# Kernel tuning notes

Measured on AMD Instinct MI355X. Metric: run time of the kernel, lower is better.

Reference implementation:

```python
import jax, jax.numpy as jnp
import numpy as np
import math

D_MODEL = 1024
NUM_HEADS = 16
HEAD_DIM = D_MODEL // NUM_HEADS
REPETITIONS = 3
NEG = -10000.0


def setup_inputs() -> dict:
    key = jax.random.key(0)
    ks = jax.random.split(key, 5)
    B, S = 2, 2048
    x = jax.random.normal(ks[0], (B, S, D_MODEL), dtype=jnp.float32)
    Wqkv_w = jax.random.normal(ks[1], (3 * D_MODEL, D_MODEL), dtype=jnp.float32) * (1.0 / math.sqrt(D_MODEL))
    Wqkv_b = jax.random.normal(ks[2], (3 * D_MODEL,), dtype=jnp.float32) * 0.02
    out_w = jax.random.normal(ks[3], (D_MODEL, D_MODEL), dtype=jnp.float32) * (1.0 / math.sqrt(D_MODEL))
    out_b = jax.random.normal(ks[4], (D_MODEL,), dtype=jnp.float32) * 0.02
    return {"x": x, "Wqkv_w": Wqkv_w, "Wqkv_b": Wqkv_b, "out_w": out_w, "out_b": out_b}


def _self_attention(q, k, v, mask):
    # q,k,v: (B,S,H,D); mask: (S,S) additive causal (-10000 above diagonal)
    scale = 1.0 / math.sqrt(q.shape[-1])
    scores = jnp.einsum('bthd,bshd->bhts', q, k * scale) + mask  # (B,H,S,S)
    attn = jax.nn.softmax(scores, axis=-1)
    return jnp.einsum('bhts,bshd->bthd', attn, v)  # (B,S,H,D)


def reference(x, Wqkv_w, Wqkv_b, out_w, out_b):
    B, S, _ = x.shape
    qkv = x @ Wqkv_w.T + Wqkv_b                       # (B,S,3*D_MODEL)
    qkv = qkv.reshape(B, S, 3, NUM_HEADS, HEAD_DIM)
    q, k, v = qkv[:, :, 0], qkv[:, :, 1], qkv[:, :, 2]
    mask = jnp.triu(jnp.full((S, S), NEG, dtype=x.dtype), 1)
    context = _self_attention(q, k, v, mask)
    # recurrent re-attention: rep_dim == 'q' -> query replaced by previous context
    for _ in range(REPETITIONS - 1):
        context = _self_attention(context, k, v, mask)
    out = context.reshape(B, S, D_MODEL) @ out_w.T + out_b
    return out
```

## Files before the change

### kernel.cpp

```cpp
#include <hip/hip_runtime.h>


#define D_MODEL 1024
#define NHEADS  16
#define HD      64
#define SEQ     2048
#define BATCH   2
#define NROWS   (BATCH*SEQ)
#define NQKV    (3*D_MODEL)
#define SCL2F   0.1803368801111601f
#define MASK2   (-14426.950408889634f)

typedef __bf16 bf16x8 __attribute__((ext_vector_type(8)));
typedef float  f32x4  __attribute__((ext_vector_type(4)));
typedef unsigned short us8 __attribute__((ext_vector_type(8)));
typedef unsigned short us4 __attribute__((ext_vector_type(4)));
typedef short  s16x4  __attribute__((ext_vector_type(4)));

__device__ __forceinline__ unsigned short f2bf(float f) {
  unsigned int u = __float_as_uint(f);
  u = (u + 0x7fffu + ((u >> 16) & 1u)) >> 16;
  return (unsigned short)u;
}

union Pack8 { us8 v; unsigned short e[8]; };
union Pack4 { us4 v; unsigned short e[4]; };

__device__ __forceinline__ us8 cvt8(const float4 &a, const float4 &b) {
  Pack8 p;
  p.e[0]=f2bf(a.x); p.e[1]=f2bf(a.y); p.e[2]=f2bf(a.z); p.e[3]=f2bf(a.w);
  p.e[4]=f2bf(b.x); p.e[5]=f2bf(b.y); p.e[6]=f2bf(b.z); p.e[7]=f2bf(b.w);
  return p.v;
}

__device__ __forceinline__ void gl_lds16(const unsigned short* g, unsigned short* l) {
  __builtin_amdgcn_global_load_lds(
      (const __attribute__((address_space(1))) unsigned int*)g,
      (__attribute__((address_space(3))) unsigned int*)l, 16, 0, 0);
}

#define CVT_N1 (NROWS*D_MODEL)
#define CVT_N2 (NQKV*D_MODEL)
#define CVT_N3 (D_MODEL*D_MODEL)

__global__ __launch_bounds__(256) void cvt_all(
    const float* __restrict__ x, const float* __restrict__ wq,
    const float* __restrict__ ow,
    unsigned short* __restrict__ xb, unsigned short* __restrict__ wqb,
    unsigned short* __restrict__ owb)
{
  size_t i = ((size_t)blockIdx.x * 256 + threadIdx.x) * 8;
  const float* src; unsigned short* dst; size_t off;
  if (i < CVT_N1)                { src = x;  dst = xb;  off = i; }
  else if (i < CVT_N1 + CVT_N2)  { src = wq; dst = wqb; off = i - CVT_N1; }
  else                           { src = ow; dst = owb; off = i - CVT_N1 - CVT_N2; }
  float4 a = *(const float4*)(src + off);
  float4 b = *(const float4*)(src + off + 4);
  *(us8*)(dst + off) = cvt8(a, b);
}

__global__ __launch_bounds__(256) void qkv_gemm(
    const unsigned short* __restrict__ xb, const unsigned short* __restrict__ wqb,
    const float* __restrict__ bias,
    unsigned short* __restrict__ q, unsigned short* __restrict__ k,
    unsigned short* __restrict__ vT)
{
  __shared__ __align__(16) unsigned short As[128*64];
  __shared__ __align__(16) unsigned short Bs[128*64];
  const int tid = threadIdx.x;
  const int m0 = blockIdx.y * 128, n0 = blockIdx.x * 128;
  const int wave = tid >> 6, lane = tid & 63;
  const int wm = (wave >> 1) * 64, wn = (wave & 1) * 64;
  const int lrow = lane & 15, quad = lane >> 4;

  const int dr = lane >> 3;
  const int pg = lane & 7;
  const int sg = (pg ^ dr) * 8;
  const unsigned short* gA[4]; const unsigned short* gB[4];
  unsigned short *lA[4], *lB[4];
  #pragma unroll
  for (int i = 0; i < 4; i++) {
    int c = wave*4 + i;
    gA[i] = xb  + (size_t)(m0 + c*8 + dr) * D_MODEL + sg;
    gB[i] = wqb + (size_t)(n0 + c*8 + dr) * D_MODEL + sg;
    lA[i] = &As[c*512];
    lB[i] = &Bs[c*512];
  }
  const int px0 = (quad ^ (lrow & 7)) * 8;
  const int px1 = ((quad + 4) ^ (lrow & 7)) * 8;

  f32x4 acc[4][4];
  #pragma unroll
  for (int i = 0; i < 4; i++)
    #pragma unroll
    for (int j = 0; j < 4; j++) acc[i][j] = (f32x4){0.f,0.f,0.f,0.f};

  for (int k0 = 0; k0 < D_MODEL; k0 += 64) {
    __syncthreads();
    #pragma unroll
    for (int i = 0; i < 4; i++) { gl_lds16(gA[i] + k0, lA[i]); gl_lds16(gB[i] + k0, lB[i]); }
    __syncthreads();
    bf16x8 af[4][2], bfr[4][2];
    #pragma unroll
    for (int mf = 0; mf < 4; mf++) {
      int row = wm + mf*16 + lrow;
      af[mf][0] = *(const bf16x8*)&As[row*64 + px0];
      af[mf][1] = *(const bf16x8*)&As[row*64 + px1];
    }
    #pragma unroll
    for (int nb = 0; nb < 4; nb++) {
      int row = wn + nb*16 + lrow;
      bfr[nb][0] = *(const bf16x8*)&Bs[row*64 + px0];
      bfr[nb][1] = *(const bf16x8*)&Bs[row*64 + px1];
    }
    #pragma unroll
    for (int h = 0; h < 2; h++)
      #pragma unroll
      for (int mf = 0; mf < 4; mf++)
        #pragma unroll
        for (int nb = 0; nb < 4; nb++)
          acc[mf][nb] = __builtin_amdgcn_mfma_f32_16x16x32_bf16(af[mf][h], bfr[nb][h], acc[mf][nb], 0, 0, 0);
  }

  #pragma unroll
  for (int mf = 0; mf < 4; mf++) {
    #pragma unroll
    for (int nb = 0; nb < 4; nb++) {
      int n = n0 + wn + nb*16 + lrow;
      int which = n >> 10;
      int h  = (n >> 6) & 15;
      int hd = n & 63;
      int mb = m0 + wm + mf*16 + quad*4;
      int b  = mb >> 11;
      int s  = mb & 2047;
      float bi = bias[n];
      if (which == 2) {
        Pack4 p4;
        #pragma unroll
        for (int r = 0; r < 4; r++) p4.e[r] = f2bf(acc[mf][nb][r] + bi);
        *(us4*)&vT[((size_t)((b*NHEADS + h)*HD + hd))*SEQ + s] = p4.v;
      } else {
        unsigned short* dst = (which == 0) ? q : k;
        float scl = (which == 0) ? SCL2F : 1.0f;
        #pragma unroll
        for (int r = 0; r < 4; r++)
          dst[(size_t)((b*NHEADS + h)*SEQ + s + r)*HD + hd] = f2bf((acc[mf][nb][r] + bi) * scl);
      }
    }
  }
}

#define LDQ 80

__global__ __launch_bounds__(256) void attn3(
    const unsigned short* __restrict__ qg,
    const unsigned short* __restrict__ kg,
    const unsigned short* __restrict__ vTg,
    unsigned short* __restrict__ ctx)
{
  __shared__ __align__(16) unsigned short Ks[2][64*LDQ];
  __shared__ __align__(16) unsigned short Vs[2][64*LDQ];
  unsigned short* QC = &Vs[0][0];

  const int tid  = threadIdx.x;
  const int w    = tid >> 6, lane = tid & 63;
  const int lrow = lane & 15, quad = lane >> 4;
  const int bh = blockIdx.x;
  const int yy = blockIdx.y;
  const int base = (blockIdx.x + yy) & 7;
  const int qt = (yy < 8) ? base : (15 - base);
  const unsigned short* qbase = qg  + (size_t)bh * SEQ * HD;
  const unsigned short* kbase = kg  + (size_t)bh * SEQ * HD;
  const unsigned short* vbase = vTg + (size_t)bh * HD * SEQ;
  unsigned short* cbase = ctx + (size_t)bh * SEQ * HD;

  const int srow = tid >> 2;
  const int sco  = (tid & 3) * 16;
  const int qrow = tid >> 1, qc0 = (tid & 1) * 32;

  {
    const unsigned short* src = qbase + (size_t)(qt*128 + qrow)*HD + qc0;
    *(uint4*)&QC[qrow*LDQ + qc0]      = *(const uint4*)src;
    *(uint4*)&QC[qrow*LDQ + qc0 + 8]  = *(const uint4*)(src + 8);
    *(uint4*)&QC[qrow*LDQ + qc0 + 16] = *(const uint4*)(src + 16);
    *(uint4*)&QC[qrow*LDQ + qc0 + 24] = *(const uint4*)(src + 24);
  }
  __syncthreads();

  bf16x8 qb[2][2];
  #pragma unroll
  for (int qgi = 0; qgi < 2; qgi++) {
    qb[qgi][0] = *(const bf16x8*)&QC[(w*32 + qgi*16 + lrow)*LDQ + quad*8];
    qb[qgi][1] = *(const bf16x8*)&QC[(w*32 + qgi*16 + lrow)*LDQ + 32 + quad*8];
  }
  __syncthreads();

  const int kmax = 2*qt + 1;
  const int qwbase = qt*128 + w*32;

  for (int rep = 0; rep < 3; ++rep) {
    f32x4 od[2][4];
    #pragma unroll
    for (int qgi = 0; qgi < 2; qgi++)
      #pragma unroll
      for (int df = 0; df < 4; df++) od[qgi][df] = (f32x4){0.f,0.f,0.f,0.f};
    float ls[2] = {0.f, 0.f};

    uint4 kr0, kr1, vr0, vr1;
    {
      const unsigned short* ks = kbase + (size_t)srow*HD + sco;
      kr0 = *(const uint4*)ks;  kr1 = *(const uint4*)(ks + 8);
      const unsigned short* vs = vbase + (size_t)srow*SEQ + sco;
      vr0 = *(const uint4*)vs;  vr1 = *(const uint4*)(vs + 8);
    }

    for (int kt = 0; kt <= kmax; ++kt) {
      const int b = kt & 1;
      *(uint4*)&Ks[b][srow*LDQ + sco]     = kr0;
      *(uint4*)&Ks[b][srow*LDQ + sco + 8] = kr1;
      *(uint4*)&Vs[b][srow*LDQ + sco]     = vr0;
      *(uint4*)&Vs[b][srow*LDQ + sco + 8] = vr1;
      if (kt < kmax) {
        const unsigned short* ks = kbase + (size_t)((kt+1)*64 + srow)*HD + sco;
        kr0 = *(const uint4*)ks;  kr1 = *(const uint4*)(ks + 8);
        const unsigned short* vs = vbase + (size_t)srow*SEQ + (kt+1)*64 + sco;
        vr0 = *(const uint4*)vs;  vr1 = *(const uint4*)(vs + 8);
      }
      __syncthreads();

      const int sbase = kt*64;
      const bool skip = sbase > (qwbase + 31);
      if (!skip) {
        f32x4 sc[2][4];
        #pragma unroll
        for (int sf = 0; sf < 4; sf++) {
          bf16x8 a0 = *(const bf16x8*)&Ks[b][(sf*16 + lrow)*LDQ + quad*8];
          bf16x8 a1 = *(const bf16x8*)&Ks[b][(sf*16 + lrow)*LDQ + 32 + quad*8];
          f32x4 z0 = (f32x4){0.f,0.f,0.f,0.f}, z1 = z0;
          z0 = __builtin_amdgcn_mfma_f32_16x16x32_bf16(a0, qb[0][0], z0, 0, 0, 0);
          z1 = __builtin_amdgcn_mfma_f32_16x16x32_bf16(a0, qb[1][0], z1, 0, 0, 0);
          z0 = __builtin_amdgcn_mfma_f32_16x16x32_bf16(a1, qb[0][1], z0, 0, 0, 0);
          z1 = __builtin_amdgcn_mfma_f32_16x16x32_bf16(a1, qb[1][1], z1, 0, 0, 0);
          sc[0][sf] = z0; sc[1][sf] = z1;
        }
        if (sbase + 63 > qwbase) {
          #pragma unroll
          for (int qgi = 0; qgi < 2; qgi++) {
            int ql = qwbase + qgi*16 + lrow;
            #pragma unroll
            for (int sf = 0; sf < 4; sf++)
              #pragma unroll
              for (int r = 0; r < 4; r++)
                if (sbase + sf*16 + quad*4 + r > ql) sc[qgi][sf][r] += MASK2;
          }
        }
        s16x4 pf[2][4];
        #pragma unroll
        for (int qgi = 0; qgi < 2; qgi++) {
          float lp = 0.f;
          #pragma unroll
          for (int sf = 0; sf < 4; sf++) {
            Pack4 pk;
            #pragma unroll
            for (int r = 0; r < 4; r++) {
              float pe = __builtin_amdgcn_exp2f(sc[qgi][sf][r]);
              lp += pe;
              pk.e[r] = __builtin_bit_cast(unsigned short, (__bf16)pe);
            }
            pf[qgi][sf] = __builtin_bit_cast(s16x4, pk.v);
          }
          ls[qgi] += lp;
        }
        #pragma unroll
        for (int df = 0; df < 4; df++) {
          s16x4 v0 = *(const s16x4*)&Vs[b][(df*16 + lrow)*LDQ +  0 + quad*4];
          s16x4 v1 = *(const s16x4*)&Vs[b][(df*16 + lrow)*LDQ + 16 + quad*4];
          s16x4 v2 = *(const s16x4*)&Vs[b][(df*16 + lrow)*LDQ + 32 + quad*4];
          s16x4 v3 = *(const s16x4*)&Vs[b][(df*16 + lrow)*LDQ + 48 + quad*4];
          od[0][df] = __builtin_amdgcn_mfma_f32_16x16x16bf16_1k(v0, pf[0][0], od[0][df], 0, 0, 0);
          od[1][df] = __builtin_amdgcn_mfma_f32_16x16x16bf16_1k(v0, pf[1][0], od[1][df], 0, 0, 0);
          od[0][df] = __builtin_amdgcn_mfma_f32_16x16x16bf16_1k(v1, pf[0][1], od[0][df], 0, 0, 0);
          od[1][df] = __builtin_amdgcn_mfma_f32_16x16x16bf16_1k(v1, pf[1][1], od[1][df], 0, 0, 0);
          od[0][df] = __builtin_amdgcn_mfma_f32_16x16x16bf16_1k(v2, pf[0][2], od[0][df], 0, 0, 0);
          od[1][df] = __builtin_amdgcn_mfma_f32_16x16x16bf16_1k(v2, pf[1][2], od[1][df], 0, 0, 0);
          od[0][df] = __builtin_amdgcn_mfma_f32_16x16x16bf16_1k(v3, pf[0][3], od[0][df], 0, 0, 0);
          od[1][df] = __builtin_amdgcn_mfma_f32_16x16x16bf16_1k(v3, pf[1][3], od[1][df], 0, 0, 0);
        }
      }
    }

    #pragma unroll
    for (int qgi = 0; qgi < 2; qgi++) {
      ls[qgi] += __shfl_xor(ls[qgi], 16);
      ls[qgi] += __shfl_xor(ls[qgi], 32);
    }

    __syncthreads();
    #pragma unroll
    for (int qgi = 0; qgi < 2; qgi++) {
      float f = ((rep < 2) ? SCL2F : 1.0f) / ls[qgi];
      #pragma unroll
      for (int df = 0; df < 4; df++) {
        Pack4 pk;
        #pragma unroll
        for (int r = 0; r < 4; r++)
          pk.e[r] = __builtin_bit_cast(unsigned short, (__bf16)(od[qgi][df][r] * f));
        *(us4*)&QC[(w*32 + qgi*16 + lrow)*LDQ + df*16 + quad*4] = pk.v;
      }
    }
    __syncthreads();
    if (rep < 2) {
      #pragma unroll
      for (int qgi = 0; qgi < 2; qgi++) {
        qb[qgi][0] = *(const bf16x8*)&QC[(w*32 + qgi*16 + lrow)*LDQ + quad*8];
        qb[qgi][1] = *(const bf16x8*)&QC[(w*32 + qgi*16 + lrow)*LDQ + 32 + quad*8];
      }
      __syncthreads();
    }
  }

  {
    unsigned short* dst = cbase + (size_t)(qt*128 + qrow)*HD + qc0;
    *(uint4*)dst        = *(const uint4*)&QC[qrow*LDQ + qc0];
    *(uint4*)(dst + 8)  = *(const uint4*)&QC[qrow*LDQ + qc0 + 8];
    *(uint4*)(dst + 16) = *(const uint4*)&QC[qrow*LDQ + qc0 + 16];
    *(uint4*)(dst + 24) = *(const uint4*)&QC[qrow*LDQ + qc0 + 24];
  }
}

__global__ __launch_bounds__(256) void out_gemm(
    const unsigned short* __restrict__ ctx, const unsigned short* __restrict__ owb,
    const float* __restrict__ bias, float* __restrict__ out)
{
  __shared__ __align__(16) unsigned short As[128*64];
  __shared__ __align__(16) unsigned short Bs[64*64];
  const int tid = threadIdx.x;
  const int m0 = blockIdx.y * 128, n0 = blockIdx.x * 64;
  const int wave = tid >> 6, lane = tid & 63;
  const int wm = (wave >> 1) * 64, wn = (wave & 1) * 32;
  const int lrow = lane & 15, quad = lane >> 4;

  const int dr = lane >> 3, pg = lane & 7;
  const int sg = (pg ^ dr) * 8;
  size_t aoff[4]; unsigned short* lA[4];
  #pragma unroll
  for (int i = 0; i < 4; i++) {
    int c = wave*4 + i;
    int row = m0 + c*8 + dr;
    aoff[i] = ((size_t)((row >> 11)*NHEADS)*SEQ + (row & 2047))*HD + sg;
    lA[i] = &As[c*512];
  }
  const unsigned short* gB[2]; unsigned short* lB[2];
  #pragma unroll
  for (int j = 0; j < 2; j++) {
    int c = wave*2 + j;
    gB[j] = owb + (size_t)(n0 + c*8 + dr) * D_MODEL + sg;
    lB[j] = &Bs[c*512];
  }
  const int px0 = (quad ^ (lrow & 7)) * 8;
  const int px1 = ((quad + 4) ^ (lrow & 7)) * 8;

  f32x4 acc[4][2];
  #pragma unroll
  for (int i = 0; i < 4; i++)
    #pragma unroll
    for (int j = 0; j < 2; j++) acc[i][j] = (f32x4){0.f,0.f,0.f,0.f};

  for (int k0 = 0; k0 < D_MODEL; k0 += 64) {
    size_t hoff = (size_t)(k0 >> 6) * SEQ * HD;
    __syncthreads();
    #pragma unroll
    for (int i = 0; i < 4; i++) gl_lds16(ctx + aoff[i] + hoff, lA[i]);
    #pragma unroll
    for (int j = 0; j < 2; j++) gl_lds16(gB[j] + k0, lB[j]);
    __syncthreads();
    bf16x8 af[4][2], bfr[2][2];
    #pragma unroll
    for (int mf = 0; mf < 4; mf++) {
      int row = wm + mf*16 + lrow;
      af[mf][0] = *(const bf16x8*)&As[row*64 + px0];
      af[mf][1] = *(const bf16x8*)&As[row*64 + px1];
    }
    #pragma unroll
    for (int nb = 0; nb < 2; nb++) {
      int row = wn + nb*16 + lrow;
      bfr[nb][0] = *(const bf16x8*)&Bs[row*64 + px0];
      bfr[nb][1] = *(const bf16x8*)&Bs[row*64 + px1];
    }
    #pragma unroll
    for (int h = 0; h < 2; h++)
      #pragma unroll
      for (int mf = 0; mf < 4; mf++)
        #pragma unroll
        for (int nb = 0; nb < 2; nb++)
          acc[mf][nb] = __builtin_amdgcn_mfma_f32_16x16x32_bf16(af[mf][h], bfr[nb][h], acc[mf][nb], 0, 0, 0);
  }

  #pragma unroll
  for (int mf = 0; mf < 4; mf++) {
    #pragma unroll
    for (int nb = 0; nb < 2; nb++) {
      #pragma unroll
      for (int r = 0; r < 4; r++) {
        int mm = m0 + wm + mf*16 + quad*4 + r;
        int n  = n0 + wn + nb*16 + lrow;
        out[(size_t)mm * D_MODEL + n] = acc[mf][nb][r] + bias[n];
      }
    }
  }
}

extern "C" void kernel_launch(void* const* d_in, const int* in_sizes, int n_in,
                              void* d_out, int out_size, void* d_ws, size_t ws_size,
                              hipStream_t stream) {
  (void)in_sizes; (void)n_in; (void)out_size; (void)ws_size;
  const float* x      = (const float*)d_in[0];
  const float* Wqkv_w = (const float*)d_in[1];
  const float* Wqkv_b = (const float*)d_in[2];
  const float* out_w  = (const float*)d_in[3];
  const float* out_b  = (const float*)d_in[4];
  float* out = (float*)d_out;

  unsigned short* ws = (unsigned short*)d_ws;
  unsigned short* xb  = ws;
  unsigned short* wqb = ws + CVT_N1;
  unsigned short* owb = ws + CVT_N1 + CVT_N2;
  unsigned short* q   = ws + CVT_N1 + CVT_N2 + CVT_N3;
  unsigned short* k   = q + (size_t)NROWS*D_MODEL;
  unsigned short* vT  = k + (size_t)NROWS*D_MODEL;
  unsigned short* ctx = xb;

  cvt_all<<<(CVT_N1+CVT_N2+CVT_N3)/(256*8), 256, 0, stream>>>(x, Wqkv_w, out_w, xb, wqb, owb);
  qkv_gemm<<<dim3(NQKV/128, NROWS/128), 256, 0, stream>>>(xb, wqb, Wqkv_b, q, k, vT);
  attn3<<<dim3(BATCH*NHEADS, SEQ/128), 256, 0, stream>>>(q, k, vT, ctx);
  out_gemm<<<dim3(D_MODEL/64, NROWS/128), 256, 0, stream>>>(ctx, owb, out_b, out);
}
```

Measured before the change: 255.5 us.

## Process key/value tiles in pairs per barrier with quad-buffered LDS

After: 246.2 us. -3.6%, faster.

```diff
diff --git a/kernel.cpp b/kernel.cpp
--- a/kernel.cpp
+++ b/kernel.cpp
@@ -150,7 +150,7 @@
   }
 }
 
-#define LDQ 80
+#define LDQ 72
 
 __global__ __launch_bounds__(256) void attn3(
     const unsigned short* __restrict__ qg,
@@ -158,8 +158,8 @@
     const unsigned short* __restrict__ vTg,
     unsigned short* __restrict__ ctx)
 {
-  __shared__ __align__(16) unsigned short Ks[2][64*LDQ];
-  __shared__ __align__(16) unsigned short Vs[2][64*LDQ];
+  __shared__ __align__(16) unsigned short Ks[4][64*LDQ];
+  __shared__ __align__(16) unsigned short Vs[4][64*LDQ];
   unsigned short* QC = &Vs[0][0];
 
   const int tid  = threadIdx.x;
@@ -195,8 +195,8 @@
   }
   __syncthreads();
 
-  const int kmax = 2*qt + 1;
   const int qwbase = qt*128 + w*32;
+  const int npair = qt + 1;
 
   for (int rep = 0; rep < 3; ++rep) {
     f32x4 od[2][4];
@@ -206,36 +206,46 @@
       for (int df = 0; df < 4; df++) od[qgi][df] = (f32x4){0.f,0.f,0.f,0.f};
     float ls[2] = {0.f, 0.f};
 
-    uint4 kr0, kr1, vr0, vr1;
+    uint4 ka0, ka1, kb0, kb1, va0, va1, vb0, vb1;
     {
       const unsigned short* ks = kbase + (size_t)srow*HD + sco;
-      kr0 = *(const uint4*)ks;  kr1 = *(const uint4*)(ks + 8);
+      ka0 = *(const uint4*)ks;  ka1 = *(const uint4*)(ks + 8);
+      kb0 = *(const uint4*)(ks + 64*HD);  kb1 = *(const uint4*)(ks + 64*HD + 8);
       const unsigned short* vs = vbase + (size_t)srow*SEQ + sco;
-      vr0 = *(const uint4*)vs;  vr1 = *(const uint4*)(vs + 8);
-    }
-
-    for (int kt = 0; kt <= kmax; ++kt) {
-      const int b = kt & 1;
-      *(uint4*)&Ks[b][srow*LDQ + sco]     = kr0;
-      *(uint4*)&Ks[b][srow*LDQ + sco + 8] = kr1;
-      *(uint4*)&Vs[b][srow*LDQ + sco]     = vr0;
-      *(uint4*)&Vs[b][srow*LDQ + sco + 8] = vr1;
-      if (kt < kmax) {
-        const unsigned short* ks = kbase + (size_t)((kt+1)*64 + srow)*HD + sco;
-        kr0 = *(const uint4*)ks;  kr1 = *(const uint4*)(ks + 8);
-        const unsigned short* vs = vbase + (size_t)srow*SEQ + (kt+1)*64 + sco;
-        vr0 = *(const uint4*)vs;  vr1 = *(const uint4*)(vs + 8);
+      va0 = *(const uint4*)vs;  va1 = *(const uint4*)(vs + 8);
+      vb0 = *(const uint4*)(vs + 64);  vb1 = *(const uint4*)(vs + 64 + 8);
+    }
+
+    for (int t = 0; t < npair; ++t) {
+      const int pb = (t & 1) * 2;
+      *(uint4*)&Ks[pb][srow*LDQ + sco]       = ka0;
+      *(uint4*)&Ks[pb][srow*LDQ + sco + 8]   = ka1;
+      *(uint4*)&Ks[pb+1][srow*LDQ + sco]     = kb0;
+      *(uint4*)&Ks[pb+1][srow*LDQ + sco + 8] = kb1;
+      *(uint4*)&Vs[pb][srow*LDQ + sco]       = va0;
+      *(uint4*)&Vs[pb][srow*LDQ + sco + 8]   = va1;
+      *(uint4*)&Vs[pb+1][srow*LDQ + sco]     = vb0;
+      *(uint4*)&Vs[pb+1][srow*LDQ + sco + 8] = vb1;
+      if (t + 1 < npair) {
+        const unsigned short* ks = kbase + (size_t)((2*t+2)*64 + srow)*HD + sco;
+        ka0 = *(const uint4*)ks;  ka1 = *(const uint4*)(ks + 8);
+        kb0 = *(const uint4*)(ks + 64*HD);  kb1 = *(const uint4*)(ks + 64*HD + 8);
+        const unsigned short* vs = vbase + (size_t)srow*SEQ + (2*t+2)*64 + sco;
+        va0 = *(const uint4*)vs;  va1 = *(const uint4*)(vs + 8);
+        vb0 = *(const uint4*)(vs + 64);  vb1 = *(const uint4*)(vs + 64 + 8);
       }
       __syncthreads();
 
-      const int sbase = kt*64;
-      const bool skip = sbase > (qwbase + 31);
-      if (!skip) {
+      #pragma unroll
+      for (int half = 0; half < 2; ++half) {
+        const int bb = pb + half;
+        const int sbase = (2*t + half) * 64;
+        if (sbase > qwbase + 31) continue;
         f32x4 sc[2][4];
         #pragma unroll
         for (int sf = 0; sf < 4; sf++) {
-          bf16x8 a0 = *(const bf16x8*)&Ks[b][(sf*16 + lrow)*LDQ + quad*8];
-          bf16x8 a1 = *(const bf16x8*)&Ks[b][(sf*16 + lrow)*LDQ + 32 + quad*8];
+          bf16x8 a0 = *(const bf16x8*)&Ks[bb][(sf*16 + lrow)*LDQ + quad*8];
+          bf16x8 a1 = *(const bf16x8*)&Ks[bb][(sf*16 + lrow)*LDQ + 32 + quad*8];
           f32x4 z0 = (f32x4){0.f,0.f,0.f,0.f}, z1 = z0;
           z0 = __builtin_amdgcn_mfma_f32_16x16x32_bf16(a0, qb[0][0], z0, 0, 0, 0);
           z1 = __builtin_amdgcn_mfma_f32_16x16x32_bf16(a0, qb[1][0], z1, 0, 0, 0);
@@ -273,10 +283,10 @@
         }
         #pragma unroll
         for (int df = 0; df < 4; df++) {
-          s16x4 v0 = *(const s16x4*)&Vs[b][(df*16 + lrow)*LDQ +  0 + quad*4];
-          s16x4 v1 = *(const s16x4*)&Vs[b][(df*16 + lrow)*LDQ + 16 + quad*4];
-          s16x4 v2 = *(const s16x4*)&Vs[b][(df*16 + lrow)*LDQ + 32 + quad*4];
-          s16x4 v3 = *(const s16x4*)&Vs[b][(df*16 + lrow)*LDQ + 48 + quad*4];
+          s16x4 v0 = *(const s16x4*)&Vs[bb][(df*16 + lrow)*LDQ +  0 + quad*4];
+          s16x4 v1 = *(const s16x4*)&Vs[bb][(df*16 + lrow)*LDQ + 16 + quad*4];
+          s16x4 v2 = *(const s16x4*)&Vs[bb][(df*16 + lrow)*LDQ + 32 + quad*4];
+          s16x4 v3 = *(const s16x4*)&Vs[bb][(df*16 + lrow)*LDQ + 48 + quad*4];
           od[0][df] = __builtin_amdgcn_mfma_f32_16x16x16bf16_1k(v0, pf[0][0], od[0][df], 0, 0, 0);
           od[1][df] = __builtin_amdgcn_mfma_f32_16x16x16bf16_1k(v0, pf[1][0], od[1][df], 0, 0, 0);
           od[0][df] = __builtin_amdgcn_mfma_f32_16x16x16bf16_1k(v1, pf[0][1], od[0][df], 0, 0, 0);
```
